# Optimization experiments

Hardware: AMD Instinct MI355X
Metric: run time of the kernel (lower is better)

The kernel has to match this reference:

```python
import jax, jax.numpy as jnp
from jax import lax
import numpy as np

SEQ_LEN, INPUT_DIM, HID, NCLS, BATCH = 1024, 1, 512, 10, 256


def setup_inputs() -> dict:
    key = jax.random.key(0)
    k1, k2, k3, k4 = jax.random.split(key, 4)
    def xavier(k, shape):
        fan_in, fan_out = shape[1], shape[0]
        bound = np.sqrt(6.0 / (fan_in + fan_out))
        return jax.random.uniform(k, shape, jnp.float32, -bound, bound)
    return {
        "x": jax.random.normal(k1, (BATCH, SEQ_LEN), jnp.float32),
        "h_init": jnp.zeros((HID, 1), jnp.float32),
        "W_hx": xavier(k2, (HID, INPUT_DIM)),
        "W_hh": xavier(k3, (HID, HID)),
        "b_h": jnp.zeros((HID, 1), jnp.float32),
        "W_ph": xavier(k4, (NCLS, HID)),
        "b_p": jnp.zeros((NCLS, 1), jnp.float32),
    }


def reference(x, h_init, W_hx, W_hh, b_h, W_ph, b_p):
    # x: [B, T] scalar inputs per step (input_dim == 1)
    B = x.shape[0]
    H = h_init.shape[0]
    # Broadcasting h_init [H,1] to [H,B] up-front is mathematically identical
    # to the torch code (W_hh @ h_init broadcasts against [H,B] at step 0).
    h0 = jnp.broadcast_to(h_init, (H, B))

    def step(h, x_t):
        # x_t: [B]; W_hx @ x_t[None,:] -> [H, B]
        h_new = jnp.tanh(W_hx @ x_t[None, :] + W_hh @ h + b_h)
        return h_new, None

    h_last, _ = lax.scan(step, h0, x.T)  # scan over time axis [T, B]
    p = W_ph @ h_last + b_p  # [NCLS, B]
    return p.T  # [B, NCLS]
```

## Files before the change

### kernel.cpp

```cpp
#include <hip/hip_runtime.h>


#define T_SEQ    1024
#define HID      512
#define NTHREADS 512
#define NW       8
#define NCLS     10
#define RP       8
#define PAIRS    32
#define PREG     26
#define PSTRIDE  576

typedef _Float16 half2_t __attribute__((ext_vector_type(2)));

__device__ __forceinline__ unsigned int pack2(float a, float b) {
    half2_t h = {(_Float16)a, (_Float16)b};
    return __builtin_bit_cast(unsigned int, h);
}

__device__ __forceinline__ float dot2(unsigned int w, unsigned int h, float acc) {
#if __has_builtin(__builtin_amdgcn_fdot2)
    return __builtin_amdgcn_fdot2(__builtin_bit_cast(half2_t, w),
                                  __builtin_bit_cast(half2_t, h), acc, false);
#else
    half2_t wv = __builtin_bit_cast(half2_t, w), hv = __builtin_bit_cast(half2_t, h);
    return acc + (float)wv.x * (float)hv.x + (float)wv.y * (float)hv.y;
#endif
}

__device__ __forceinline__ unsigned int bcast(unsigned int v, int lane) {
#if __has_builtin(__builtin_amdgcn_readlane)
    return __builtin_amdgcn_readlane(v, lane);
#else
    return __shfl((int)v, lane, 64);
#endif
}

__device__ __forceinline__ int pidx(int row) { return row + ((row >> 5) << 2); }

__device__ __forceinline__ float fast_tanh(float s) {
#if __has_builtin(__builtin_amdgcn_exp2f)
    float e = __builtin_amdgcn_exp2f(s * 2.885390081777927f);
#else
    float e = __expf(2.0f * s);
#endif
    return 1.0f - 2.0f / (e + 1.0f);
}

__global__ __attribute__((amdgpu_flat_work_group_size(NTHREADS, NTHREADS)))
           __attribute__((amdgpu_waves_per_eu(2, 2)))
void rnn_persist(
    const float* __restrict__ x, const float* __restrict__ h_init,
    const float* __restrict__ W_hx, const float* __restrict__ W_hh,
    const float* __restrict__ b_h, const float* __restrict__ W_ph,
    const float* __restrict__ b_p, float* __restrict__ out)
{
    __shared__ uint4  Wl4[NW * RP * 64];
    __shared__ uint2  Wl2[NW * RP * 64];
    __shared__ float  part[2][NW][PSTRIDE];
    __shared__ float  x_s[T_SEQ];

    const int tid  = threadIdx.x;
    const int b    = blockIdx.x;
    const int w    = tid >> 6;
    const int lane = tid & 63;

    for (int i = tid; i < T_SEQ; i += NTHREADS) x_s[i] = x[(size_t)b * T_SEQ + i];

    const int  r0c  = 64 * w + 2 * (lane & 31);
    const float whx0 = W_hx[r0c],     bh0 = b_h[r0c];
    const float whx1 = W_hx[r0c + 1], bh1 = b_h[r0c + 1];
    const int  pi   = pidx(r0c);

    unsigned int wreg[RP][PREG];
    #pragma unroll
    for (int r = 0; r < RP; ++r) {
        const float4* row = (const float4*)(W_hh + (size_t)(RP * lane + r) * HID + 64 * w);
        #pragma unroll
        for (int q = 0; q < 13; ++q) {
            float4 v = row[q];
            wreg[r][2 * q]     = pack2(v.x, v.y);
            wreg[r][2 * q + 1] = pack2(v.z, v.w);
        }
        float4 v13 = row[13], v14 = row[14], v15 = row[15];
        Wl4[(w * RP + r) * 64 + lane] =
            make_uint4(pack2(v13.x, v13.y), pack2(v13.z, v13.w),
                       pack2(v14.x, v14.y), pack2(v14.z, v14.w));
        Wl2[(w * RP + r) * 64 + lane] =
            make_uint2(pack2(v15.x, v15.y), pack2(v15.z, v15.w));
#if __has_builtin(__builtin_amdgcn_sched_barrier)
        __builtin_amdgcn_sched_barrier(0);
#endif
    }

    #pragma unroll
    for (int r = 0; r < RP; ++r)
        #pragma unroll
        for (int p = 0; p < PREG; ++p)
            asm volatile("" : "+v"(wreg[r][p]));

    __syncthreads();

    float h0 = 0.0f, h1 = 0.0f;
    unsigned int hpack = pack2(h_init[r0c], h_init[r0c + 1]);

    #pragma unroll 1
    for (int t = 0; t < T_SEQ; ++t) {
        const int buf = t & 1;
        const float xw = x_s[t];

        float acc[RP];
        #pragma unroll
        for (int r = 0; r < RP; ++r) acc[r] = 0.0f;

        #pragma unroll
        for (int p = 0; p < PREG; ++p) {
            unsigned int hp = bcast(hpack, p);
            #pragma unroll
            for (int r = 0; r < RP; ++r) acc[r] = dot2(wreg[r][p], hp, acc[r]);
        }
        {
            unsigned int hh0 = bcast(hpack, 26), hh1 = bcast(hpack, 27),
                         hh2 = bcast(hpack, 28), hh3 = bcast(hpack, 29),
                         hh4 = bcast(hpack, 30), hh5 = bcast(hpack, 31);
            #pragma unroll
            for (int r = 0; r < RP; ++r) {
                uint4 wq = Wl4[(w * RP + r) * 64 + lane];
                uint2 wd = Wl2[(w * RP + r) * 64 + lane];
                acc[r] = dot2(wq.x, hh0, acc[r]);
                acc[r] = dot2(wq.y, hh1, acc[r]);
                acc[r] = dot2(wq.z, hh2, acc[r]);
                acc[r] = dot2(wq.w, hh3, acc[r]);
                acc[r] = dot2(wd.x, hh4, acc[r]);
                acc[r] = dot2(wd.y, hh5, acc[r]);
            }
        }

        *(float4*)&part[buf][w][pidx(RP * lane)]     = make_float4(acc[0], acc[1], acc[2], acc[3]);
        *(float4*)&part[buf][w][pidx(RP * lane + 4)] = make_float4(acc[4], acc[5], acc[6], acc[7]);

        __syncthreads();

        float s0 = whx0 * xw + bh0;
        float s1 = whx1 * xw + bh1;
        #pragma unroll
        for (int j = 0; j < NW; ++j) {
            float2 pv = *(const float2*)&part[buf][j][pi];
            s0 += pv.x;
            s1 += pv.y;
        }
        h0 = fast_tanh(s0);
        h1 = fast_tanh(s1);
        hpack = pack2(h0, h1);
    }

    __syncthreads();
    if (lane < 32) {
        x_s[r0c]     = h0;
        x_s[r0c + 1] = h1;
    }
    __syncthreads();

    for (int c = w; c < NCLS; c += NW) {
        float s = 0.0f;
        #pragma unroll
        for (int j = 0; j < 8; ++j) {
            int r = lane + 64 * j;
            s += W_ph[c * HID + r] * x_s[r];
        }
        #pragma unroll
        for (int off = 32; off; off >>= 1) s += __shfl_down(s, off, 64);
        if (lane == 0) out[b * NCLS + c] = s + b_p[c];
    }
}

extern "C" void kernel_launch(void* const* d_in, const int* in_sizes, int n_in,
                              void* d_out, int out_size, void* d_ws, size_t ws_size,
                              hipStream_t stream) {
    const float* x      = (const float*)d_in[0];
    const float* h_init = (const float*)d_in[1];
    const float* W_hx   = (const float*)d_in[2];
    const float* W_hh   = (const float*)d_in[3];
    const float* b_h    = (const float*)d_in[4];
    const float* W_ph   = (const float*)d_in[5];
    const float* b_p    = (const float*)d_in[6];
    float* out = (float*)d_out;

    const int B = in_sizes[0] / T_SEQ;
    rnn_persist<<<B, NTHREADS, 0, stream>>>(x, h_init, W_hx, W_hh, b_h, W_ph, b_p, out);
}
```

Measured before the change: 1.667 ms.

## Keep more W_hh pairs in registers and compute one hidden unit per thread

Raises the number of packed W_hh half2 pairs held per thread in registers from 26 to 28. This leaves only one uint4 per row in LDS and drops the uint2 LDS weight array along with its per-step reads. The tanh/reduction stage now gives each thread one hidden unit instead of two duplicated across half-waves. The new h value is passed through a small fp16 LDS buffer that the same wave reads back at the next step. The cost is higher VGPR pressure (about 224 weight registers), which risks spills, plus an extra LDS write and read per step.

```diff
diff --git a/kernel.cpp b/kernel.cpp
--- a/kernel.cpp
+++ b/kernel.cpp
@@ -8,7 +8,7 @@
 #define NCLS     10
 #define RP       8
 #define PAIRS    32
-#define PREG     26
+#define PREG     28
 #define PSTRIDE  576
 
 typedef _Float16 half2_t __attribute__((ext_vector_type(2)));
@@ -55,10 +55,10 @@
     const float* __restrict__ b_h, const float* __restrict__ W_ph,
     const float* __restrict__ b_p, float* __restrict__ out)
 {
-    __shared__ uint4  Wl4[NW * RP * 64];
-    __shared__ uint2  Wl2[NW * RP * 64];
-    __shared__ float  part[2][NW][PSTRIDE];
-    __shared__ float  x_s[T_SEQ];
+    __shared__ uint4    Wl4[NW * RP * 64];
+    __shared__ float    part[2][NW][PSTRIDE];
+    __shared__ float    x_s[T_SEQ];
+    __shared__ _Float16 hs[HID];
 
     const int tid  = threadIdx.x;
     const int b    = blockIdx.x;
@@ -67,27 +67,34 @@
 
     for (int i = tid; i < T_SEQ; i += NTHREADS) x_s[i] = x[(size_t)b * T_SEQ + i];
 
-    const int  r0c  = 64 * w + 2 * (lane & 31);
-    const float whx0 = W_hx[r0c],     bh0 = b_h[r0c];
-    const float whx1 = W_hx[r0c + 1], bh1 = b_h[r0c + 1];
-    const int  pi   = pidx(r0c);
+    const float whx = W_hx[tid];
+    const float bh  = b_h[tid];
+    const int   pi  = pidx(tid);
+    hs[tid] = (_Float16)h_init[tid];
 
     unsigned int wreg[RP][PREG];
     #pragma unroll
     for (int r = 0; r < RP; ++r) {
         const float4* row = (const float4*)(W_hh + (size_t)(RP * lane + r) * HID + 64 * w);
         #pragma unroll
-        for (int q = 0; q < 13; ++q) {
+        for (int q = 0; q < 7; ++q) {
             float4 v = row[q];
             wreg[r][2 * q]     = pack2(v.x, v.y);
             wreg[r][2 * q + 1] = pack2(v.z, v.w);
         }
-        float4 v13 = row[13], v14 = row[14], v15 = row[15];
+#if __has_builtin(__builtin_amdgcn_sched_barrier)
+        __builtin_amdgcn_sched_barrier(0);
+#endif
+        #pragma unroll
+        for (int q = 7; q < 14; ++q) {
+            float4 v = row[q];
+            wreg[r][2 * q]     = pack2(v.x, v.y);
+            wreg[r][2 * q + 1] = pack2(v.z, v.w);
+        }
+        float4 v14 = row[14], v15 = row[15];
         Wl4[(w * RP + r) * 64 + lane] =
-            make_uint4(pack2(v13.x, v13.y), pack2(v13.z, v13.w),
-                       pack2(v14.x, v14.y), pack2(v14.z, v14.w));
-        Wl2[(w * RP + r) * 64 + lane] =
-            make_uint2(pack2(v15.x, v15.y), pack2(v15.z, v15.w));
+            make_uint4(pack2(v14.x, v14.y), pack2(v14.z, v14.w),
+                       pack2(v15.x, v15.y), pack2(v15.z, v15.w));
 #if __has_builtin(__builtin_amdgcn_sched_barrier)
         __builtin_amdgcn_sched_barrier(0);
 #endif
@@ -101,13 +108,15 @@
 
     __syncthreads();
 
-    float h0 = 0.0f, h1 = 0.0f;
-    unsigned int hpack = pack2(h_init[r0c], h_init[r0c + 1]);
+    const unsigned int* hs32 = (const unsigned int*)hs;
+    float hval = 0.0f;
 
     #pragma unroll 1
     for (int t = 0; t < T_SEQ; ++t) {
         const int buf = t & 1;
         const float xw = x_s[t];
+
+        unsigned int hpack = hs32[w * 32 + (lane & 31)];
 
         float acc[RP];
         #pragma unroll
@@ -120,19 +129,15 @@
             for (int r = 0; r < RP; ++r) acc[r] = dot2(wreg[r][p], hp, acc[r]);
         }
         {
-            unsigned int hh0 = bcast(hpack, 26), hh1 = bcast(hpack, 27),
-                         hh2 = bcast(hpack, 28), hh3 = bcast(hpack, 29),
-                         hh4 = bcast(hpack, 30), hh5 = bcast(hpack, 31);
+            unsigned int hh0 = bcast(hpack, 28), hh1 = bcast(hpack, 29),
+                         hh2 = bcast(hpack, 30), hh3 = bcast(hpack, 31);
             #pragma unroll
             for (int r = 0; r < RP; ++r) {
                 uint4 wq = Wl4[(w * RP + r) * 64 + lane];
-                uint2 wd = Wl2[(w * RP + r) * 64 + lane];
                 acc[r] = dot2(wq.x, hh0, acc[r]);
                 acc[r] = dot2(wq.y, hh1, acc[r]);
                 acc[r] = dot2(wq.z, hh2, acc[r]);
                 acc[r] = dot2(wq.w, hh3, acc[r]);
-                acc[r] = dot2(wd.x, hh4, acc[r]);
-                acc[r] = dot2(wd.y, hh5, acc[r]);
             }
         }
 
@@ -141,24 +146,16 @@
 
         __syncthreads();
 
-        float s0 = whx0 * xw + bh0;
-        float s1 = whx1 * xw + bh1;
+        float s = whx * xw + bh;
         #pragma unroll
-        for (int j = 0; j < NW; ++j) {
-            float2 pv = *(const float2*)&part[buf][j][pi];
-            s0 += pv.x;
-            s1 += pv.y;
-        }
-        h0 = fast_tanh(s0);
-        h1 = fast_tanh(s1);
-        hpack = pack2(h0, h1);
+        for (int j = 0; j < NW; ++j) s += part[buf][j][pi];
+
+        hval = fast_tanh(s);
+        hs[tid] = (_Float16)hval;
     }
 
     __syncthreads();
-    if (lane < 32) {
-        x_s[r0c]     = h0;
-        x_s[r0c + 1] = h1;
-    }
+    x_s[tid] = hval;
     __syncthreads();
 
     for (int c = w; c < NCLS; c += NW) {
```

New measurement: 1.436 ms (median of 2 runs). 1.16x faster.
